# Optimization experiments

Hardware: AMD Instinct MI355X
Metric: run time of the kernel (lower is better)

## Reference

```python
import jax, jax.numpy as jnp
import numpy as np


def setup_inputs() -> dict:
    key = jax.random.key(0)
    k1, k2, k3 = jax.random.split(key, 3)
    bs, S, d, C = 2, 196, 512, 1006
    imgFeaturemap = jax.random.normal(k1, (bs, S, d), dtype=jnp.float32)
    wordFeatures = jax.random.normal(k2, (C, d), dtype=jnp.float32)
    fc3_w = jax.random.normal(k3, (d, d), dtype=jnp.float32) * 0.02
    fc3_b = jnp.zeros((d,), dtype=jnp.float32)
    return {"imgFeaturemap": imgFeaturemap, "wordFeatures": wordFeatures,
            "fc3_w": fc3_w, "fc3_b": fc3_b}


def reference(imgFeaturemap, wordFeatures, fc3_w, fc3_b):
    # imgFeaturemap: (bs, S, d); wordFeatures: (C, d)
    # Broadcast multiply + tanh: (bs, S, C, d)
    t = jnp.tanh(imgFeaturemap[:, :, None, :] * wordFeatures[None, None, :, :])
    # Per-row Linear (PyTorch Linear: x @ W^T + b)
    feat = jnp.einsum('bscd,ed->bsce', t, fc3_w) + fc3_b
    # Softmax over spatial axis S (axis=1), independently per (class, channel)
    coef = jax.nn.softmax(feat, axis=1)
    # Softmax-weighted spatial pooling per class: (bs, C, d)
    semanticFeature = jnp.einsum('bsd,bscd->bcd', imgFeaturemap, coef)
    return semanticFeature
```

## Files before the change

kernel.cpp:

```cpp
#include <hip/hip_runtime.h>

using half8   = __attribute__((ext_vector_type(8))) _Float16;
using floatx4 = __attribute__((ext_vector_type(4))) float;

namespace {
constexpr int S = 196, D = 512, C = 1006, Cpad = 1024;
constexpr int CB = 16;
constexpr int EBLK = 256;
constexpr int BK = 64;
constexpr int TPB = 256;
constexpr int SCH = 3;
constexpr int RS = 64;
constexpr float KTANH = 2.885390082f;
constexpr float INVK  = 0.34657359028f;
constexpr float LOG2E = 1.44269504f;

constexpr size_t W16_BYTES = (size_t)D * D * 2;
constexpr size_t LA_OFF    = W16_BYTES;
constexpr size_t SLICE_ELEMS = (size_t)2 * Cpad * D;
constexpr size_t SL_BYTES  = (size_t)SCH * SLICE_ELEMS * 4;
constexpr size_t SLICE_NEED = LA_OFF + 2 * SL_BYTES;
constexpr size_t L_BYTES   = SLICE_ELEMS * 4;

__device__ __forceinline__ int sw_off(int row, int seg) {
    return row * RS + ((seg ^ (row & 7)) << 3);
}

__device__ __forceinline__ void gload16(const _Float16* g, _Float16* l) {
    __builtin_amdgcn_global_load_lds(
        (const __attribute__((address_space(1))) unsigned int*)g,
        (__attribute__((address_space(3))) unsigned int*)l, 16, 0, 0);
}

__device__ __forceinline__ _Float16 tanh_ps(float y) {
    float e = __builtin_amdgcn_exp2f(y);
    return (_Float16)(1.0f - 2.0f * __builtin_amdgcn_rcpf(e + 1.0f));
}

__global__ void prep_w16sw(const float* __restrict__ fw, _Float16* __restrict__ W16sw) {
    int id = blockIdx.x * blockDim.x + threadIdx.x;
    int kki = id >> 12;
    int r   = (id >> 3) & 511;
    int j   = id & 7;
    const float* src = fw + (size_t)r * D + kki * BK + j * 8;
    floatx4 v0 = *(const floatx4*)src;
    floatx4 v1 = *(const floatx4*)(src + 4);
    half8 h;
    h[0] = (_Float16)(v0[0] * LOG2E); h[1] = (_Float16)(v0[1] * LOG2E);
    h[2] = (_Float16)(v0[2] * LOG2E); h[3] = (_Float16)(v0[3] * LOG2E);
    h[4] = (_Float16)(v1[0] * LOG2E); h[5] = (_Float16)(v1[1] * LOG2E);
    h[6] = (_Float16)(v1[2] * LOG2E); h[7] = (_Float16)(v1[3] * LOG2E);
    *(half8*)&W16sw[((size_t)kki << 15) + r * RS + ((j ^ (r & 7)) << 3)] = h;
}

__global__ __launch_bounds__(TPB, 3) void semdec_mfma(
    const float* __restrict__ img, const float* __restrict__ word,
    const _Float16* __restrict__ W16sw,
    float* __restrict__ lbase, float* __restrict__ abase, int use_slice)
{
    __shared__ __align__(16) _Float16 Wc[EBLK * RS];
    __shared__ __align__(16) _Float16 Tc[4 * CB * RS];
    __shared__ __align__(16) float imgS[4][D];

    const int ct = blockIdx.x;
    const int et = blockIdx.y & 1;
    const int b  = blockIdx.y >> 1;
    const int sc = blockIdx.z;

    const int tid  = threadIdx.x;
    const int lane = tid & 63;
    const int wv   = tid >> 6;
    const int l15  = lane & 15;
    const int quad = lane >> 4;

    const int c0 = ct * CB;
    const int e0 = et * EBLK;

    const int siB  = tid >> 7;
    const int ciT  = (tid & 127) >> 3;
    const int segT = tid & 7;
    int cgT = c0 + ciT; if (cgT > C - 1) cgT = C - 1;
    const float* wordRowT = word + (size_t)cgT * D + segT * 8;

    floatx4 lacc[4], aacc[4];
    #pragma unroll
    for (int ej = 0; ej < 4; ++ej) {
        lacc[ej] = (floatx4){0.f, 0.f, 0.f, 0.f};
        aacc[ej] = (floatx4){0.f, 0.f, 0.f, 0.f};
    }

    const float* imgB = img + (size_t)b * S * D;
    const int s_base = sc * 66;
    const int npass = (sc < 2) ? 17 : 16;

    floatx4 wc0 = *(const floatx4*)(wordRowT);
    floatx4 wc1 = *(const floatx4*)(wordRowT + 4);

    for (int pr = 0; pr < npass; ++pr) {
        const int s0 = s_base + pr * 4;
        const int slim = (pr == 16) ? 2 : 4;

        __syncthreads();
        #pragma unroll
        for (int it = 0; it < 2; ++it) {
            int sid = it * TPB + tid;
            int si = sid >> 7, pos = (sid & 127) << 2;
            floatx4 v = *(const floatx4*)&imgB[(size_t)(s0 + si) * D + pos];
            floatx4 sv = {v[0] * KTANH, v[1] * KTANH, v[2] * KTANH, v[3] * KTANH};
            *(floatx4*)&imgS[si][pos] = sv;
        }

        floatx4 acc[4][4];
        #pragma unroll
        for (int si = 0; si < 4; ++si)
            #pragma unroll
            for (int ej = 0; ej < 4; ++ej)
                acc[si][ej] = (floatx4){0.f, 0.f, 0.f, 0.f};

        for (int kk = 0; kk < D; kk += BK) {
            const int kki = kk >> 6;
            __syncthreads();
            {
                const _Float16* wg = W16sw + ((size_t)kki << 15) + ((size_t)e0 << 6);
                #pragma unroll
                for (int it = 0; it < 8; ++it) {
                    int o = ((wv * 8 + it) << 9) + (lane << 3);
                    gload16(wg + o, &Wc[o]);
                }
            }
            #pragma unroll
            for (int it = 0; it < 2; ++it) {
                int si = it * 2 + siB;
                const float* ip = &imgS[si][kk + segT * 8];
                floatx4 i0 = *(const floatx4*)ip;
                floatx4 i1 = *(const floatx4*)(ip + 4);
                half8 t;
                t[0] = tanh_ps(i0[0] * wc0[0]); t[1] = tanh_ps(i0[1] * wc0[1]);
                t[2] = tanh_ps(i0[2] * wc0[2]); t[3] = tanh_ps(i0[3] * wc0[3]);
                t[4] = tanh_ps(i1[0] * wc1[0]); t[5] = tanh_ps(i1[1] * wc1[1]);
                t[6] = tanh_ps(i1[2] * wc1[2]); t[7] = tanh_ps(i1[3] * wc1[3]);
                *(half8*)&Tc[sw_off(si * CB + ciT, segT)] = t;
            }
            __syncthreads();

            const int knext = (kk + BK) & (D - 1);
            floatx4 wn0 = *(const floatx4*)(wordRowT + knext);
            floatx4 wn1 = *(const floatx4*)(wordRowT + knext + 4);

            #pragma unroll
            for (int k2 = 0; k2 < 2; ++k2) {
                const int jb = (k2 << 2) + quad;
                half8 bf[4], af[4];
                #pragma unroll
                for (int ej = 0; ej < 4; ++ej)
                    bf[ej] = *(const half8*)&Wc[sw_off(wv * 64 + ej * 16 + l15, jb)];
                #pragma unroll
                for (int si = 0; si < 4; ++si)
                    af[si] = *(const half8*)&Tc[sw_off(si * CB + l15, jb)];
                #pragma unroll
                for (int si = 0; si < 4; ++si)
                    #pragma unroll
                    for (int ej = 0; ej < 4; ++ej)
                        acc[si][ej] = __builtin_amdgcn_mfma_f32_16x16x32_f16(
                            af[si], bf[ej], acc[si][ej], 0, 0, 0);
            }
            wc0 = wn0; wc1 = wn1;
        }
        #pragma unroll
        for (int si = 0; si < 4; ++si) {
            if (si >= slim) break;
            #pragma unroll
            for (int ej = 0; ej < 4; ++ej) {
                float ie = imgS[si][e0 + wv * 64 + ej * 16 + l15] * INVK;
                #pragma unroll
                for (int r = 0; r < 4; ++r) {
                    float ev = __builtin_amdgcn_exp2f(acc[si][ej][r]);
                    lacc[ej][r] += ev;
                    aacc[ej][r] += ie * ev;
                }
            }
        }
    }

    if (use_slice) {
        float* lsl = lbase + (size_t)sc * SLICE_ELEMS;
        float* asl = abase + (size_t)sc * SLICE_ELEMS;
        #pragma unroll
        for (int r = 0; r < 4; ++r) {
            int cg = c0 + quad * 4 + r;
            #pragma unroll
            for (int ej = 0; ej < 4; ++ej) {
                int eg = e0 + wv * 64 + ej * 16 + l15;
                size_t o = ((size_t)b * Cpad + cg) * D + eg;
                lsl[o] = lacc[ej][r];
                asl[o] = aacc[ej][r];
            }
        }
    } else {
        #pragma unroll
        for (int r = 0; r < 4; ++r) {
            int cg = c0 + quad * 4 + r;
            #pragma unroll
            for (int ej = 0; ej < 4; ++ej) {
                int eg = e0 + wv * 64 + ej * 16 + l15;
                atomicAdd(&lbase[((size_t)b * Cpad + cg) * D + eg], lacc[ej][r]);
                if (cg < C)
                    atomicAdd(&abase[((size_t)b * C + cg) * D + eg], aacc[ej][r]);
            }
        }
    }
}

__global__ void finalize_k(const float* __restrict__ lbase, const float* __restrict__ abase,
                           float* __restrict__ out, int use_slice) {
    int o = blockIdx.x * blockDim.x + threadIdx.x;
    if (o >= 2 * C * D) return;
    int b = o / (C * D);
    int rem = o - b * (C * D);
    int c = rem >> 9;
    int e = rem & (D - 1);
    size_t p = ((size_t)b * Cpad + c) * D + e;
    if (use_slice) {
        float l = 0.f, a = 0.f;
        #pragma unroll
        for (int scn = 0; scn < SCH; ++scn) {
            l += lbase[(size_t)scn * SLICE_ELEMS + p];
            a += abase[(size_t)scn * SLICE_ELEMS + p];
        }
        out[o] = a / l;
    } else {
        out[o] = out[o] / lbase[p];
    }
}

}

extern "C" void kernel_launch(void* const* d_in, const int* in_sizes, int n_in,
                              void* d_out, int out_size, void* d_ws, size_t ws_size,
                              hipStream_t stream) {
    const float* img  = (const float*)d_in[0];
    const float* word = (const float*)d_in[1];
    const float* fw   = (const float*)d_in[2];
    float* out = (float*)d_out;
    char* ws = (char*)d_ws;

    _Float16* W16sw = (_Float16*)ws;
    const int use_slice = (ws_size >= SLICE_NEED) ? 1 : 0;

    hipLaunchKernelGGL(prep_w16sw, dim3(128), dim3(256), 0, stream, fw, W16sw);

    float *lbase, *abase;
    if (use_slice) {
        lbase = (float*)(ws + LA_OFF);
        abase = (float*)(ws + LA_OFF + SL_BYTES);
    } else {
        lbase = (float*)(ws + LA_OFF);
        abase = out;
        hipMemsetAsync(lbase, 0, L_BYTES, stream);
        hipMemsetAsync(out, 0, (size_t)2 * C * D * 4, stream);
    }

    hipLaunchKernelGGL(semdec_mfma, dim3(64, 4, SCH), dim3(TPB), 0, stream,
                       img, word, W16sw, lbase, abase, use_slice);

    hipLaunchKernelGGL(finalize_k, dim3((2 * C * D + 255) / 256), dim3(256), 0, stream,
                       lbase, abase, out, use_slice);
}
```

Baseline: 360.8 us.

## Cover all E per block, read W fragments from global, double-buffer tanh tile

Each block now spans all 512 output channels with 8 waves instead of splitting E across two blocks, so the tanh tile is computed once per (class, spatial) group rather than twice. The W tile is no longer staged in LDS; MFMA B fragments are read straight from the pre-swizzled global (L2-resident) half buffer. The tanh tile is double-buffered so the next K-chunk's tanh runs between the fragment loads and the MFMAs, which removes one barrier per K step. Spatial chunks drop from 3 to 2, giving fewer blocks with more registers each, and the final partial pass clamps its row index.

```diff
diff --git a/kernel.cpp b/kernel.cpp
--- a/kernel.cpp
+++ b/kernel.cpp
@@ -5,36 +5,38 @@
 
 namespace {
 constexpr int S = 196, D = 512, C = 1006, Cpad = 1024;
-constexpr int CB = 16;
-constexpr int EBLK = 256;
-constexpr int BK = 64;
-constexpr int TPB = 256;
-constexpr int SCH = 3;
-constexpr int RS = 64;
+constexpr int CB  = 16;
+constexpr int BK  = 64;
+constexpr int TPB = 512;
+constexpr int SCH = 2;
+constexpr int RS  = 64;
 constexpr float KTANH = 2.885390082f;
 constexpr float INVK  = 0.34657359028f;
 constexpr float LOG2E = 1.44269504f;
 
-constexpr size_t W16_BYTES = (size_t)D * D * 2;
-constexpr size_t LA_OFF    = W16_BYTES;
+constexpr size_t W16_BYTES   = (size_t)D * D * 2;
+constexpr size_t LA_OFF      = W16_BYTES;
 constexpr size_t SLICE_ELEMS = (size_t)2 * Cpad * D;
-constexpr size_t SL_BYTES  = (size_t)SCH * SLICE_ELEMS * 4;
-constexpr size_t SLICE_NEED = LA_OFF + 2 * SL_BYTES;
-constexpr size_t L_BYTES   = SLICE_ELEMS * 4;
+constexpr size_t SL_BYTES    = (size_t)SCH * SLICE_ELEMS * 4;
+constexpr size_t SLICE_NEED  = LA_OFF + 2 * SL_BYTES;
+constexpr size_t L_BYTES     = SLICE_ELEMS * 4;
 
 __device__ __forceinline__ int sw_off(int row, int seg) {
     return row * RS + ((seg ^ (row & 7)) << 3);
-}
-
-__device__ __forceinline__ void gload16(const _Float16* g, _Float16* l) {
-    __builtin_amdgcn_global_load_lds(
-        (const __attribute__((address_space(1))) unsigned int*)g,
-        (__attribute__((address_space(3))) unsigned int*)l, 16, 0, 0);
 }
 
 __device__ __forceinline__ _Float16 tanh_ps(float y) {
     float e = __builtin_amdgcn_exp2f(y);
     return (_Float16)(1.0f - 2.0f * __builtin_amdgcn_rcpf(e + 1.0f));
+}
+
+__device__ __forceinline__ half8 tanh8(floatx4 i0, floatx4 i1, floatx4 w0, floatx4 w1) {
+    half8 t;
+    t[0] = tanh_ps(i0[0] * w0[0]); t[1] = tanh_ps(i0[1] * w0[1]);
+    t[2] = tanh_ps(i0[2] * w0[2]); t[3] = tanh_ps(i0[3] * w0[3]);
+    t[4] = tanh_ps(i1[0] * w1[0]); t[5] = tanh_ps(i1[1] * w1[1]);
+    t[6] = tanh_ps(i1[2] * w1[2]); t[7] = tanh_ps(i1[3] * w1[3]);
+    return t;
 }
 
 __global__ void prep_w16sw(const float* __restrict__ fw, _Float16* __restrict__ W16sw) {
@@ -53,18 +55,16 @@
     *(half8*)&W16sw[((size_t)kki << 15) + r * RS + ((j ^ (r & 7)) << 3)] = h;
 }
 
-__global__ __launch_bounds__(TPB, 3) void semdec_mfma(
+__global__ __launch_bounds__(TPB, 2) void semdec_mfma(
     const float* __restrict__ img, const float* __restrict__ word,
     const _Float16* __restrict__ W16sw,
     float* __restrict__ lbase, float* __restrict__ abase, int use_slice)
 {
-    __shared__ __align__(16) _Float16 Wc[EBLK * RS];
-    __shared__ __align__(16) _Float16 Tc[4 * CB * RS];
+    __shared__ __align__(16) _Float16 Tc[2][4 * CB * RS];
     __shared__ __align__(16) float imgS[4][D];
 
     const int ct = blockIdx.x;
-    const int et = blockIdx.y & 1;
-    const int b  = blockIdx.y >> 1;
+    const int b  = blockIdx.y;
     const int sc = blockIdx.z;
 
     const int tid  = threadIdx.x;
@@ -74,10 +74,9 @@
     const int quad = lane >> 4;
 
     const int c0 = ct * CB;
-    const int e0 = et * EBLK;
-
-    const int siB  = tid >> 7;
-    const int ciT  = (tid & 127) >> 3;
+
+    const int siT  = tid >> 7;
+    const int ciT  = (tid >> 3) & 15;
     const int segT = tid & 7;
     int cgT = c0 + ciT; if (cgT > C - 1) cgT = C - 1;
     const float* wordRowT = word + (size_t)cgT * D + segT * 8;
@@ -90,25 +89,35 @@
     }
 
     const float* imgB = img + (size_t)b * S * D;
-    const int s_base = sc * 66;
-    const int npass = (sc < 2) ? 17 : 16;
+    const int s_base = sc * 98;
+    constexpr int NPASS = 25;
 
     floatx4 wc0 = *(const floatx4*)(wordRowT);
     floatx4 wc1 = *(const floatx4*)(wordRowT + 4);
-
-    for (int pr = 0; pr < npass; ++pr) {
+    floatx4 wn0 = *(const floatx4*)(wordRowT + BK);
+    floatx4 wn1 = *(const floatx4*)(wordRowT + BK + 4);
+
+    for (int pr = 0; pr < NPASS; ++pr) {
         const int s0 = s_base + pr * 4;
-        const int slim = (pr == 16) ? 2 : 4;
+        const int slim = (pr == NPASS - 1) ? 2 : 4;
 
         __syncthreads();
-        #pragma unroll
-        for (int it = 0; it < 2; ++it) {
-            int sid = it * TPB + tid;
-            int si = sid >> 7, pos = (sid & 127) << 2;
-            floatx4 v = *(const floatx4*)&imgB[(size_t)(s0 + si) * D + pos];
-            floatx4 sv = {v[0] * KTANH, v[1] * KTANH, v[2] * KTANH, v[3] * KTANH};
-            *(floatx4*)&imgS[si][pos] = sv;
-        }
+        {
+            int si = tid >> 7, pos = (tid & 127) << 2;
+            int srow = s0 + si; if (srow > S - 1) srow = S - 1;
+            floatx4 v = *(const floatx4*)&imgB[(size_t)srow * D + pos];
+            *(floatx4*)&imgS[si][pos] = v * KTANH;
+        }
+        __syncthreads();
+
+        {
+            const float* ip = &imgS[siT][segT * 8];
+            floatx4 i0 = *(const floatx4*)ip;
+            floatx4 i1 = *(const floatx4*)(ip + 4);
+            *(half8*)&Tc[0][sw_off(siT * CB + ciT, segT)] = tanh8(i0, i1, wc0, wc1);
+        }
+        wc0 = wn0; wc1 = wn1;
+        __syncthreads();
 
         floatx4 acc[4][4];
         #pragma unroll
@@ -117,61 +126,56 @@
             for (int ej = 0; ej < 4; ++ej)
                 acc[si][ej] = (floatx4){0.f, 0.f, 0.f, 0.f};
 
-        for (int kk = 0; kk < D; kk += BK) {
-            const int kki = kk >> 6;
-            __syncthreads();
+        for (int kk = 0; kk < 8; ++kk) {
+            const int p = kk & 1;
+            const _Float16* Tcp = Tc[p];
+
+            const _Float16* wgk = W16sw + ((size_t)kk << 15);
+            half8 bf[2][4], af[2][4];
+            #pragma unroll
+            for (int k2 = 0; k2 < 2; ++k2)
+                #pragma unroll
+                for (int ej = 0; ej < 4; ++ej)
+                    bf[k2][ej] = *(const half8*)&wgk[sw_off(wv * 64 + ej * 16 + l15, (k2 << 2) + quad)];
+
             {
-                const _Float16* wg = W16sw + ((size_t)kki << 15) + ((size_t)e0 << 6);
-                #pragma unroll
-                for (int it = 0; it < 8; ++it) {
-                    int o = ((wv * 8 + it) << 9) + (lane << 3);
-                    gload16(wg + o, &Wc[o]);
-                }
-            }
-            #pragma unroll
-            for (int it = 0; it < 2; ++it) {
-                int si = it * 2 + siB;
-                const float* ip = &imgS[si][kk + segT * 8];
+                const int kc = ((kk + 2) & 7) * BK;
+                wn0 = *(const floatx4*)(wordRowT + kc);
+                wn1 = *(const floatx4*)(wordRowT + kc + 4);
+            }
+
+            #pragma unroll
+            for (int k2 = 0; k2 < 2; ++k2)
+                #pragma unroll
+                for (int si = 0; si < 4; ++si)
+                    af[k2][si] = *(const half8*)&Tcp[sw_off(si * CB + l15, (k2 << 2) + quad)];
+
+            if (kk < 7) {
+                const float* ip = &imgS[siT][((kk + 1) << 6) + segT * 8];
                 floatx4 i0 = *(const floatx4*)ip;
                 floatx4 i1 = *(const floatx4*)(ip + 4);
-                half8 t;
-                t[0] = tanh_ps(i0[0] * wc0[0]); t[1] = tanh_ps(i0[1] * wc0[1]);
-                t[2] = tanh_ps(i0[2] * wc0[2]); t[3] = tanh_ps(i0[3] * wc0[3]);
-                t[4] = tanh_ps(i1[0] * wc1[0]); t[5] = tanh_ps(i1[1] * wc1[1]);
-                t[6] = tanh_ps(i1[2] * wc1[2]); t[7] = tanh_ps(i1[3] * wc1[3]);
-                *(half8*)&Tc[sw_off(si * CB + ciT, segT)] = t;
-            }
-            __syncthreads();
-
-            const int knext = (kk + BK) & (D - 1);
-            floatx4 wn0 = *(const floatx4*)(wordRowT + knext);
-            floatx4 wn1 = *(const floatx4*)(wordRowT + knext + 4);
-
-            #pragma unroll
-            for (int k2 = 0; k2 < 2; ++k2) {
-                const int jb = (k2 << 2) + quad;
-                half8 bf[4], af[4];
-                #pragma unroll
-                for (int ej = 0; ej < 4; ++ej)
-                    bf[ej] = *(const half8*)&Wc[sw_off(wv * 64 + ej * 16 + l15, jb)];
-                #pragma unroll
-                for (int si = 0; si < 4; ++si)
-                    af[si] = *(const half8*)&Tc[sw_off(si * CB + l15, jb)];
+                *(half8*)&Tc[p ^ 1][sw_off(siT * CB + ciT, segT)] = tanh8(i0, i1, wc0, wc1);
+                wc0 = wn0; wc1 = wn1;
+            }
+
+            #pragma unroll
+            for (int k2 = 0; k2 < 2; ++k2)
                 #pragma unroll
                 for (int si = 0; si < 4; ++si)
                     #pragma unroll
                     for (int ej = 0; ej < 4; ++ej)
                         acc[si][ej] = __builtin_amdgcn_mfma_f32_16x16x32_f16(
-                            af[si], bf[ej], acc[si][ej], 0, 0, 0);
-            }
-            wc0 = wn0; wc1 = wn1;
-        }
+                            af[k2][si], bf[k2][ej], acc[si][ej], 0, 0, 0);
+
+            __syncthreads();
+        }
+
         #pragma unroll
         for (int si = 0; si < 4; ++si) {
             if (si >= slim) break;
             #pragma unroll
             for (int ej = 0; ej < 4; ++ej) {
-                float ie = imgS[si][e0 + wv * 64 + ej * 16 + l15] * INVK;
+                float ie = imgS[si][wv * 64 + ej * 16 + l15] * INVK;
                 #pragma unroll
                 for (int r = 0; r < 4; ++r) {
                     float ev = __builtin_amdgcn_exp2f(acc[si][ej][r]);
@@ -190,7 +194,7 @@
             int cg = c0 + quad * 4 + r;
             #pragma unroll
             for (int ej = 0; ej < 4; ++ej) {
-                int eg = e0 + wv * 64 + ej * 16 + l15;
+                int eg = wv * 64 + ej * 16 + l15;
                 size_t o = ((size_t)b * Cpad + cg) * D + eg;
                 lsl[o] = lacc[ej][r];
                 asl[o] = aacc[ej][r];
@@ -202,7 +206,7 @@
             int cg = c0 + quad * 4 + r;
             #pragma unroll
             for (int ej = 0; ej < 4; ++ej) {
-                int eg = e0 + wv * 64 + ej * 16 + l15;
+                int eg = wv * 64 + ej * 16 + l15;
                 atomicAdd(&lbase[((size_t)b * Cpad + cg) * D + eg], lacc[ej][r]);
                 if (cg < C)
                     atomicAdd(&abase[((size_t)b * C + cg) * D + eg], aacc[ej][r]);
@@ -260,7 +264,7 @@
         hipMemsetAsync(out, 0, (size_t)2 * C * D * 4, stream);
     }
 
-    hipLaunchKernelGGL(semdec_mfma, dim3(64, 4, SCH), dim3(TPB), 0, stream,
+    hipLaunchKernelGGL(semdec_mfma, dim3(64, 2, SCH), dim3(TPB), 0, stream,
                        img, word, W16sw, lbase, abase, use_slice);
 
     hipLaunchKernelGGL(finalize_k, dim3((2 * C * D + 255) / 256), dim3(256), 0, stream,
```

After: 569.5 us. 57.9% more time.
